# Kernel optimization log

Hardware: AMD Instinct MI355X
Metric: run time of the kernel (lower is better)

## Reference

```python
import jax, jax.numpy as jnp
import numpy as np

N, E, D, G, L = 100_000, 500_000, 128, 512, 4
BN_EPS = 1e-5

def _bn(v, g, b):
    # BatchNorm1d in training mode: biased batch stats over node/graph axis
    m = v.mean(0)
    var = v.var(0)
    return (v - m) * jax.lax.rsqrt(var + BN_EPS) * g + b

def setup_inputs() -> dict:
    key = jax.random.key(0)
    ks = jax.random.split(key, 12)
    s = 0.05
    return {
        "x": jax.random.normal(ks[0], (N, D), jnp.float32),
        "edge_index": jax.random.randint(ks[1], (2, E), 0, N, jnp.int64),
        "batch": jnp.sort(jax.random.randint(ks[2], (N,), 0, G, jnp.int64)),
        "num_graphs": G,
        "W1": jax.random.normal(ks[3], (L, D, 2 * D), jnp.float32) * s,
        "b1": jnp.zeros((L, 2 * D), jnp.float32),
        "g1": jnp.ones((L, 2 * D), jnp.float32),
        "be1": jnp.zeros((L, 2 * D), jnp.float32),
        "W2": jax.random.normal(ks[4], (L, 2 * D, D), jnp.float32) * s,
        "b2": jnp.zeros((L, D), jnp.float32),
        "gbn": jnp.ones((L, D), jnp.float32),
        "bbn": jnp.zeros((L, D), jnp.float32),
        "eps": jnp.zeros((L,), jnp.float32),
        "cW1": jax.random.normal(ks[5], (3 * D, D), jnp.float32) * s,
        "cb1": jnp.zeros((D,), jnp.float32),
        "cg": jnp.ones((D,), jnp.float32),
        "cbeta": jnp.zeros((D,), jnp.float32),
        "cW2": jax.random.normal(ks[6], (D, D // 2), jnp.float32) * s,
        "cb2": jnp.zeros((D // 2,), jnp.float32),
        "cW3": jax.random.normal(ks[7], (D // 2, 2), jnp.float32) * s,
        "cb3": jnp.zeros((2,), jnp.float32),
    }

def reference(x, edge_index, batch, num_graphs, W1, b1, g1, be1, W2, b2, gbn, bbn, eps,
              cW1, cb1, cg, cbeta, cW2, cb2, cW3, cb3):
    n = x.shape[0]
    src, dst = edge_index[0], edge_index[1]
    for l in range(W1.shape[0]):
        # GINConv: mlp((1+eps)*x + sum_{j in N(i)} x_j)  (scatter-add to dst)
        agg = jax.ops.segment_sum(x[src], dst, num_segments=n)
        h = (1.0 + eps[l]) * x + agg
        h = jax.nn.relu(_bn(h @ W1[l] + b1[l], g1[l], be1[l]))
        h = h @ W2[l] + b2[l]
        x = jax.nn.relu(_bn(h, gbn[l], bbn[l]))  # outer BN + ReLU (dropout off: eval)
    # multi-pool readout: add / mean / max per graph
    s = jax.ops.segment_sum(x, batch, num_segments=num_graphs)
    cnt = jax.ops.segment_sum(jnp.ones((n,), x.dtype), batch, num_segments=num_graphs)
    mean = s / jnp.maximum(cnt, 1.0)[:, None]
    mx = jax.ops.segment_max(x, batch, num_segments=num_graphs)
    z = jnp.concatenate([s, mean, mx], axis=-1)  # [G, 3*D]
    z = jax.nn.relu(_bn(z @ cW1 + cb1, cg, cbeta))
    z = jax.nn.relu(z @ cW2 + cb2)
    return z @ cW3 + cb3
```

## Files before the change

kernel.cpp:

```cpp
#include <hip/hip_runtime.h>
#include <cstdint>
#include <cstddef>

#define NN 100000
#define EE 500000
#define DD 128
#define GG 512
#define LL 4
#define BN_EPS 1e-5f

typedef __attribute__((ext_vector_type(8))) short short8;
typedef __attribute__((ext_vector_type(8))) unsigned short ushort8v;
typedef __attribute__((ext_vector_type(4))) float f32x4;

static __device__ __forceinline__ unsigned short f2bf(float f) {
  union { float f; unsigned u; } v;
  v.f = f;
  unsigned r = v.u + 0x7fffu + ((v.u >> 16) & 1u);
  return (unsigned short)(r >> 16);
}
static __device__ __forceinline__ float bf2f(unsigned short u) {
  union { unsigned u; float f; } v;
  v.u = ((unsigned)u) << 16;
  return v.f;
}


__global__ void k_hist(const int* __restrict__ ei, int* __restrict__ cnt) {
  int e = blockIdx.x * 256 + threadIdx.x;
  if (e < EE) {
    int d = ei[EE + e];
    if (d >= 0 && d < NN) atomicAdd(&cnt[d], 1);
  }
}

__global__ void k_part(const int* __restrict__ cnt, int* __restrict__ part) {
  __shared__ int sm[1024];
  int t = threadIdx.x;
  int i = blockIdx.x * 1024 + t;
  sm[t] = (i < NN) ? cnt[i] : 0;
  __syncthreads();
  for (int off = 512; off > 0; off >>= 1) {
    if (t < off) sm[t] += sm[t + off];
    __syncthreads();
  }
  if (t == 0) part[blockIdx.x] = sm[0];
}

__global__ void k_scanpart(const int* __restrict__ part, int* __restrict__ partx, int nb) {
  __shared__ int sm[128];
  int t = threadIdx.x;
  int v = (t < nb) ? part[t] : 0;
  sm[t] = v;
  __syncthreads();
  for (int off = 1; off < 128; off <<= 1) {
    int u = (t >= off) ? sm[t - off] : 0;
    __syncthreads();
    sm[t] += u;
    __syncthreads();
  }
  if (t < nb) partx[t] = sm[t] - v;
}

__global__ void k_rs(const int* __restrict__ cnt, const int* __restrict__ partx,
                     int* __restrict__ rs, int* __restrict__ cur) {
  __shared__ int sm[1024];
  int t = threadIdx.x;
  int i = blockIdx.x * 1024 + t;
  int v = (i < NN) ? cnt[i] : 0;
  sm[t] = v;
  __syncthreads();
  for (int off = 1; off < 1024; off <<= 1) {
    int u = (t >= off) ? sm[t - off] : 0;
    __syncthreads();
    sm[t] += u;
    __syncthreads();
  }
  if (i < NN) {
    int excl = partx[blockIdx.x] + sm[t] - v;
    rs[i] = excl;
    cur[i] = excl;
    if (i == NN - 1) rs[NN] = excl + v;
  }
}

__global__ void k_fill(const int* __restrict__ ei, int* __restrict__ cur,
                       int* __restrict__ ci) {
  int e = blockIdx.x * 256 + threadIdx.x;
  if (e < EE) {
    int s = ei[e];
    int d = ei[EE + e];
    if (d >= 0 && d < NN && s >= 0 && s < NN) {
      int pos = atomicAdd(&cur[d], 1);
      if (pos >= 0 && pos < EE) ci[pos] = s;
    }
  }
}


__global__ void k_conv(const float* __restrict__ W1, const float* __restrict__ W2,
                       unsigned short* __restrict__ W1t, unsigned short* __restrict__ W2t) {
  int idx = blockIdx.x * 256 + threadIdx.x;
  if (idx < 4 * 256 * 128) {
    {
      int l = idx >> 15, rem = idx & 32767;
      int nc = rem >> 7, k = rem & 127;
      W1t[idx] = f2bf(W1[(l << 15) + k * 256 + nc]);
    }
    {
      int l = idx >> 15, rem = idx & 32767;
      int nc = rem >> 8, k = rem & 255;
      W2t[idx] = f2bf(W2[(l << 15) + k * 128 + nc]);
    }
  }
}


__global__ void k_x2bf(const float* __restrict__ x, unsigned short* __restrict__ xb) {
  int i = blockIdx.x * 256 + threadIdx.x;
  if (i < NN * DD / 4) {
    float4 v = *(const float4*)(x + (size_t)i * 4);
    ushort4 o;
    o.x = f2bf(v.x); o.y = f2bf(v.y); o.z = f2bf(v.z); o.w = f2bf(v.w);
    *(ushort4*)(xb + (size_t)i * 4) = o;
  }
}


__global__ __launch_bounds__(256) void k_agg_bf16(
    const unsigned short* __restrict__ X, const int* __restrict__ rs,
    const int* __restrict__ ci, const float* __restrict__ epsv, int l, int mode,
    const float* __restrict__ tsc, const float* __restrict__ tsh,
    unsigned short* __restrict__ h0, int n) {
  int idx = blockIdx.x * 256 + threadIdx.x;
  int node = idx >> 4;
  int c8 = (idx & 15) << 3;
  if (node >= n) return;
  float sa[8], sb[8];
  if (mode) {
    float4 a0 = *(const float4*)(tsc + c8), a1 = *(const float4*)(tsc + c8 + 4);
    float4 b0 = *(const float4*)(tsh + c8), b1 = *(const float4*)(tsh + c8 + 4);
    sa[0] = a0.x; sa[1] = a0.y; sa[2] = a0.z; sa[3] = a0.w;
    sa[4] = a1.x; sa[5] = a1.y; sa[6] = a1.z; sa[7] = a1.w;
    sb[0] = b0.x; sb[1] = b0.y; sb[2] = b0.z; sb[3] = b0.w;
    sb[4] = b1.x; sb[5] = b1.y; sb[6] = b1.z; sb[7] = b1.w;
  }
  float se = 1.f + epsv[l];
  ushort8v v = *(const ushort8v*)(X + (size_t)node * DD + c8);
  float acc[8];
#pragma unroll
  for (int j = 0; j < 8; ++j) {
    float f = bf2f(v[j]);
    if (mode) f = fmaxf(0.f, f * sa[j] + sb[j]);
    acc[j] = se * f;
  }
  int e0 = rs[node], e1 = rs[node + 1];
  ushort8v un;
  if (e0 < e1) un = *(const ushort8v*)(X + (size_t)ci[e0] * DD + c8);
  for (int e = e0; e < e1; ++e) {
    ushort8v uc = un;
    if (e + 1 < e1) un = *(const ushort8v*)(X + (size_t)ci[e + 1] * DD + c8);
#pragma unroll
    for (int j = 0; j < 8; ++j) {
      float f = bf2f(uc[j]);
      if (mode) f = fmaxf(0.f, f * sa[j] + sb[j]);
      acc[j] += f;
    }
  }
  ushort8v o;
#pragma unroll
  for (int j = 0; j < 8; ++j) o[j] = f2bf(acc[j]);
  *(ushort8v*)(h0 + (size_t)node * DD + c8) = o;
}


__global__ __launch_bounds__(512) void k_mom(
    const unsigned short* __restrict__ h0, float* __restrict__ M2s,
    float* __restrict__ css, int n) {
  constexpr int HT = 264;
  __shared__ __align__(16) unsigned short Ht[128 * HT];
  __shared__ float lcs[128];
  int tid = threadIdx.x;
  int lane = tid & 63, wave = tid >> 6;
  int quad = lane >> 4, l15 = lane & 15;
  int n0 = blockIdx.x * 256;
  if (tid < 128) lcs[tid] = 0.f;
  int c8 = (tid & 15) << 3;
  int rloc = tid >> 4;
  float csr[8];
#pragma unroll
  for (int j = 0; j < 8; ++j) csr[j] = 0.f;
  __syncthreads();
#pragma unroll
  for (int pass = 0; pass < 8; ++pass) {
    int nl = rloc + pass * 32;
    int gr = n0 + nl;
    ushort8v v = (ushort8v){0, 0, 0, 0, 0, 0, 0, 0};
    if (gr < n) v = *(const ushort8v*)(h0 + (size_t)gr * DD + c8);
#pragma unroll
    for (int j = 0; j < 8; ++j) {
      Ht[(c8 + j) * HT + nl] = v[j];
      csr[j] += bf2f(v[j]);
    }
  }
#pragma unroll
  for (int j = 0; j < 8; ++j) atomicAdd(&lcs[c8 + j], csr[j]);
  __syncthreads();
  f32x4 acc[8];
#pragma unroll
  for (int j = 0; j < 8; ++j) acc[j] = (f32x4){0.f, 0.f, 0.f, 0.f};
#pragma unroll
  for (int kc = 0; kc < 8; ++kc) {
    int ko = kc * 32 + quad * 8;
    short8 av = *(const short8*)(&Ht[(wave * 16 + l15) * HT + ko]);
#pragma unroll
    for (int j = 0; j < 8; ++j) {
      short8 bv = *(const short8*)(&Ht[(j * 16 + l15) * HT + ko]);
      acc[j] = __builtin_amdgcn_mfma_f32_16x16x32_bf16(av, bv, acc[j], 0, 0, 0);
    }
  }
  int slab = blockIdx.x & 7;
  float* M2 = M2s + (size_t)slab * (128 * 128);
  int lr = wave * 16 + quad * 4;
#pragma unroll
  for (int j = 0; j < 8; ++j)
#pragma unroll
    for (int reg = 0; reg < 4; ++reg)
      atomicAdd(&M2[(lr + reg) * 128 + j * 16 + l15], acc[j][reg]);
  if (tid < 128) atomicAdd(&css[slab * 128 + tid], lcs[tid]);
}

__global__ void k_red(const float* __restrict__ M2s, const float* __restrict__ css,
                      float* __restrict__ M2f, float* __restrict__ csf) {
  int i = blockIdx.x * 256 + threadIdx.x;
  float s = 0.f;
#pragma unroll
  for (int k = 0; k < 8; ++k) s += M2s[(size_t)k * 16384 + i];
  M2f[i] = s;
  if (i < 128) {
    float c = 0.f;
#pragma unroll
    for (int k = 0; k < 8; ++k) c += css[k * 128 + i];
    csf[i] = c;
  }
}

__global__ __launch_bounds__(128) void k_bn1(
    const float* __restrict__ M2, const float* __restrict__ cs,
    const unsigned short* __restrict__ W1t_l, const float* __restrict__ g1_l,
    const float* __restrict__ be1_l, float* __restrict__ osc,
    float* __restrict__ osh) {
  __shared__ float wsh[128];
  __shared__ float red1[2], red2[2];
  int c = blockIdx.x, t = threadIdx.x;
  float w = bf2f(W1t_l[c * 128 + t]);
  wsh[t] = w;
  __syncthreads();
  float inner = 0.f;
#pragma unroll 4
  for (int k = 0; k < 128; ++k) inner = fmaf(M2[t * 128 + k], wsh[k], inner);
  float s1 = w * inner;
  float s2 = w * cs[t];
#pragma unroll
  for (int off = 32; off > 0; off >>= 1) {
    s1 += __shfl_xor(s1, off, 64);
    s2 += __shfl_xor(s2, off, 64);
  }
  if ((t & 63) == 0) { red1[t >> 6] = s1; red2[t >> 6] = s2; }
  __syncthreads();
  if (t == 0) {
    float q = (red1[0] + red1[1]) * (1.0f / NN);
    float um = (red2[0] + red2[1]) * (1.0f / NN);
    float var = fmaxf(q - um * um, 0.f);
    float sc = g1_l[c] * rsqrtf(var + BN_EPS);
    osc[c] = sc;
    osh[c] = be1_l[c] - um * sc;
  }
}


__global__ __launch_bounds__(512, 4) void k_gfused(
    const unsigned short* __restrict__ A, const float* __restrict__ sc1,
    const float* __restrict__ sh1, const unsigned short* __restrict__ W1t_l,
    const unsigned short* __restrict__ W2t_l, const float* __restrict__ b2_l,
    unsigned short* __restrict__ C, float* __restrict__ psum,
    float* __restrict__ psq, int n) {
  constexpr int AST = 72;
  constexpr int HP = 136;
  __shared__ __align__(16) unsigned short smem[2 * 128 * AST];
  __shared__ __align__(16) unsigned short H[128 * HP];
  __shared__ float bsum[128], bsq[128];
  unsigned short* Asm = smem;
  unsigned short* Bsm = smem + 128 * AST;

  int tid = threadIdx.x;
  int lane = tid & 63, wave = tid >> 6;
  int quad = lane >> 4, l15 = lane & 15;
  int row0 = blockIdx.x * 128;

  ushort8v pa[2], pb[2];
  f32x4 acc1[8], acc2[8];
#pragma unroll
  for (int j = 0; j < 8; ++j) acc2[j] = (f32x4){0.f, 0.f, 0.f, 0.f};

#define LOADS1(cg, kc)                                                         \
  {                                                                            \
    _Pragma("unroll") for (int it = 0; it < 2; ++it) {                         \
      int f = tid + it * 512, rr = f >> 3, c8 = (f & 7) << 3;                  \
      int gr = row0 + rr;                                                      \
      pa[it] = (ushort8v){0, 0, 0, 0, 0, 0, 0, 0};                             \
      if (gr < n)                                                              \
        pa[it] = *(const ushort8v*)(A + (size_t)gr * 128 + (kc)*64 + c8);      \
      pb[it] = *(const ushort8v*)(W1t_l +                                      \
                                  (size_t)((cg)*128 + rr) * 128 + (kc)*64 + c8); \
    }                                                                          \
  }
#define LOADS2(kc2)                                                            \
  {                                                                            \
    _Pragma("unroll") for (int it = 0; it < 2; ++it) {                         \
      int f = tid + it * 512, rr = f >> 3, c8 = (f & 7) << 3;                  \
      pb[it] = *(const ushort8v*)(W2t_l + (size_t)rr * 256 + (kc2)*64 + c8);   \
    }                                                                          \
  }
#define WRITES1                                                                \
  {                                                                            \
    _Pragma("unroll") for (int it = 0; it < 2; ++it) {                         \
      int f = tid + it * 512, rr = f >> 3, c8 = (f & 7) << 3;                  \
      *(ushort8v*)(&Asm[rr * AST + c8]) = pa[it];                              \
      *(ushort8v*)(&Bsm[rr * AST + c8]) = pb[it];                              \
    }                                                                          \
  }
#define WRITES2                                                                \
  {                                                                            \
    _Pragma("unroll") for (int it = 0; it < 2; ++it) {                         \
      int f = tid + it * 512, rr = f >> 3, c8 = (f & 7) << 3;                  \
      *(ushort8v*)(&Bsm[rr * AST + c8]) = pb[it];                              \
    }                                                                          \
  }
#define ZERO1                                                                  \
  {                                                                            \
    _Pragma("unroll") for (int j = 0; j < 8; ++j)                              \
        acc1[j] = (f32x4){0.f, 0.f, 0.f, 0.f};                                 \
  }
#define MFMAS1                                                                 \
  {                                                                            \
    _Pragma("unroll") for (int kk = 0; kk < 64; kk += 32) {                    \
      int ko = kk + quad * 8;                                                  \
      short8 av = *(const short8*)(&Asm[(wave * 16 + l15) * AST + ko]);        \
      _Pragma("unroll") for (int cf = 0; cf < 8; ++cf) {                       \
        short8 bv = *(const short8*)(&Bsm[(cf * 16 + l15) * AST + ko]);        \
        acc1[cf] =                                                             \
            __builtin_amdgcn_mfma_f32_16x16x32_bf16(av, bv, acc1[cf], 0, 0, 0); \
      }                                                                        \
    }                                                                          \
  }
#define MFMAS2(half)                                                           \
  {                                                                            \
    _Pragma("unroll") for (int kk = 0; kk < 64; kk += 32) {                    \
      int ko = kk + quad * 8;                                                  \
      short8 av =                                                              \
          *(const short8*)(&H[(wave * 16 + l15) * HP + (half)*64 + ko]);       \
      _Pragma("unroll") for (int cf = 0; cf < 8; ++cf) {                       \
        short8 bv = *(const short8*)(&Bsm[(cf * 16 + l15) * AST + ko]);        \
        acc2[cf] =                                                             \
            __builtin_amdgcn_mfma_f32_16x16x32_bf16(av, bv, acc2[cf], 0, 0, 0); \
      }                                                                        \
    }                                                                          \
  }
#define EPI1(cg)                                                               \
  {                                                                            \
    int lrb = wave * 16 + quad * 4;                                            \
    _Pragma("unroll") for (int cf = 0; cf < 8; ++cf) {                         \
      int col = (cg)*128 + cf * 16 + l15;                                      \
      float sc = sc1[col], sh = sh1[col];                                      \
      _Pragma("unroll") for (int reg = 0; reg < 4; ++reg)                      \
          H[(lrb + reg) * HP + cf * 16 + l15] =                                \
              f2bf(fmaxf(0.f, acc1[cf][reg] * sc + sh));                       \
    }                                                                          \
  }

  LOADS1(0, 0)
  WRITES1 __syncthreads();
  LOADS1(0, 1) ZERO1 MFMAS1 __syncthreads();
  WRITES1 __syncthreads();
  LOADS2(0) MFMAS1 EPI1(0) __syncthreads();
  WRITES2 __syncthreads();
  LOADS2(1) MFMAS2(0) __syncthreads();
  WRITES2 __syncthreads();
  LOADS1(1, 0) MFMAS2(1) __syncthreads();
  WRITES1 __syncthreads();
  LOADS1(1, 1) ZERO1 MFMAS1 __syncthreads();
  WRITES1 __syncthreads();
  LOADS2(2) MFMAS1 EPI1(1) __syncthreads();
  WRITES2 __syncthreads();
  LOADS2(3) MFMAS2(0) __syncthreads();
  WRITES2 __syncthreads();
  MFMAS2(1)

  __syncthreads();
  unsigned short* Ct = smem;
  if (tid < 128) { bsum[tid] = 0.f; bsq[tid] = 0.f; }
  float s8[8], q8[8];
#pragma unroll
  for (int j = 0; j < 8; ++j) { s8[j] = 0.f; q8[j] = 0.f; }
  int lrbase = wave * 16 + quad * 4;
#pragma unroll
  for (int cf = 0; cf < 8; ++cf) {
    float bv = b2_l[cf * 16 + l15];
#pragma unroll
    for (int reg = 0; reg < 4; ++reg) {
      int lr = lrbase + reg;
      float e = acc2[cf][reg] + bv;
      Ct[lr * HP + cf * 16 + l15] = f2bf(e);
      if (row0 + lr < n) { s8[cf] += e; q8[cf] += e * e; }
    }
  }
#pragma unroll
  for (int cf = 0; cf < 8; ++cf) {
    s8[cf] += __shfl_xor(s8[cf], 16, 64);
    s8[cf] += __shfl_xor(s8[cf], 32, 64);
    q8[cf] += __shfl_xor(q8[cf], 16, 64);
    q8[cf] += __shfl_xor(q8[cf], 32, 64);
  }
  __syncthreads();
  if (quad == 0) {
#pragma unroll
    for (int cf = 0; cf < 8; ++cf) {
      atomicAdd(&bsum[cf * 16 + l15], s8[cf]);
      atomicAdd(&bsq[cf * 16 + l15], q8[cf]);
    }
  }
#pragma unroll
  for (int it = 0; it < 4; ++it) {
    int f = tid + it * 512;
    int r = f >> 4, c8 = (f & 15) << 3;
    int gr = row0 + r;
    if (gr < n)
      *(ushort8v*)(C + (size_t)gr * 128 + c8) = *(const ushort8v*)(&Ct[r * HP + c8]);
  }
  __syncthreads();
  if (tid < 128) {
    psum[(size_t)blockIdx.x * 128 + tid] = bsum[tid];
    psq[(size_t)blockIdx.x * 128 + tid] = bsq[tid];
  }
#undef LOADS1
#undef LOADS2
#undef WRITES1
#undef WRITES2
#undef ZERO1
#undef MFMAS1
#undef MFMAS2
#undef EPI1
}


__global__ __launch_bounds__(256) void k_finred(
    const float* __restrict__ psum, const float* __restrict__ psq, int nb, int nc,
    const float* __restrict__ g, const float* __restrict__ be,
    float* __restrict__ osc, float* __restrict__ osh, float invn) {
  __shared__ float ws[4], wq[4];
  int col = blockIdx.x;
  int t = threadIdx.x;
  float s = 0.f, q = 0.f;
  for (int b = t; b < nb; b += 256) {
    s += psum[(size_t)b * nc + col];
    q += psq[(size_t)b * nc + col];
  }
#pragma unroll
  for (int off = 32; off > 0; off >>= 1) {
    s += __shfl_xor(s, off, 64);
    q += __shfl_xor(q, off, 64);
  }
  if ((t & 63) == 0) { ws[t >> 6] = s; wq[t >> 6] = q; }
  __syncthreads();
  if (t == 0) {
    s = ws[0] + ws[1] + ws[2] + ws[3];
    q = wq[0] + wq[1] + wq[2] + wq[3];
    float m = s * invn;
    float v = fmaxf(q * invn - m * m, 0.f);
    float sc = g[col] * rsqrtf(v + BN_EPS);
    osc[col] = sc;
    osh[col] = be[col] - m * sc;
  }
}


__global__ __launch_bounds__(256) void k_statz(
    const float* __restrict__ z1, const float* __restrict__ g,
    const float* __restrict__ be, float* __restrict__ osc, float* __restrict__ osh) {
  __shared__ float ws[4], wq[4];
  int col = blockIdx.x;
  int t = threadIdx.x;
  float s = 0.f, q = 0.f;
  for (int b = t; b < GG; b += 256) {
    float v = z1[(size_t)b * 128 + col];
    s += v;
    q += v * v;
  }
#pragma unroll
  for (int off = 32; off > 0; off >>= 1) {
    s += __shfl_xor(s, off, 64);
    q += __shfl_xor(q, off, 64);
  }
  if ((t & 63) == 0) { ws[t >> 6] = s; wq[t >> 6] = q; }
  __syncthreads();
  if (t == 0) {
    s = ws[0] + ws[1] + ws[2] + ws[3];
    q = wq[0] + wq[1] + wq[2] + wq[3];
    float m = s / (float)GG;
    float v = fmaxf(q / (float)GG - m * m, 0.f);
    float sc = g[col] * rsqrtf(v + BN_EPS);
    osc[col] = sc;
    osh[col] = be[col] - m * sc;
  }
}


static __device__ __forceinline__ int lb_i32(const int* a, int n, int key) {
  int lo = 0, hi = n;
  while (lo < hi) {
    int mid = (lo + hi) >> 1;
    if (a[mid] < key) lo = mid + 1; else hi = mid;
  }
  return lo;
}

__global__ __launch_bounds__(512) void k_pool(
    const unsigned short* __restrict__ X, const int* __restrict__ batch,
    const float* __restrict__ tsc, const float* __restrict__ tsh,
    float* __restrict__ z, int n) {
  __shared__ int slo, shi;
  __shared__ float ssum[8][128], smax[8][128];
  int g = blockIdx.x;
  int t = threadIdx.x;
  int sg = t >> 6;
  int c2 = (t & 63) << 1;
  if (t == 0) {
    slo = lb_i32(batch, n, g);
    shi = lb_i32(batch, n, g + 1);
  }
  __syncthreads();
  int lo = slo, hi = shi;
  float a0 = tsc[c2], a1 = tsc[c2 + 1];
  float b0 = tsh[c2], b1 = tsh[c2 + 1];
  float s0 = 0.f, s1 = 0.f;
  float m0 = -3.402823466e38f, m1 = -3.402823466e38f;
  for (int i = lo + sg; i < hi; i += 8) {
    unsigned u = *(const unsigned*)(X + (size_t)i * DD + c2);
    float v0 = fmaxf(0.f, bf2f((unsigned short)(u & 0xffff)) * a0 + b0);
    float v1 = fmaxf(0.f, bf2f((unsigned short)(u >> 16)) * a1 + b1);
    s0 += v0; m0 = fmaxf(m0, v0);
    s1 += v1; m1 = fmaxf(m1, v1);
  }
  ssum[sg][c2] = s0; ssum[sg][c2 + 1] = s1;
  smax[sg][c2] = m0; smax[sg][c2 + 1] = m1;
  __syncthreads();
  if (t < 128) {
    float S = 0.f, M = -3.402823466e38f;
#pragma unroll
    for (int k = 0; k < 8; ++k) {
      S += ssum[k][t];
      M = fmaxf(M, smax[k][t]);
    }
    float cntf = (float)(hi - lo);
    z[(size_t)g * 384 + t] = S;
    z[(size_t)g * 384 + 128 + t] = S / fmaxf(cntf, 1.f);
    z[(size_t)g * 384 + 256 + t] = M;
  }
}


__global__ void k_cls1(const float* __restrict__ z, const float* __restrict__ cW1,
                       const float* __restrict__ cb1, float* __restrict__ z1) {
  __shared__ float zr[384];
  int g = blockIdx.x;
  int c = threadIdx.x;
  for (int i = c; i < 384; i += 128) zr[i] = z[(size_t)g * 384 + i];
  __syncthreads();
  float s = cb1[c];
#pragma unroll 4
  for (int k = 0; k < 384; ++k) s = fmaf(zr[k], cW1[(size_t)k * 128 + c], s);
  z1[(size_t)g * 128 + c] = s;
}

__global__ void k_cls2(const float* __restrict__ z1, const float* __restrict__ csc,
                       const float* __restrict__ csh, const float* __restrict__ cW2,
                       const float* __restrict__ cb2, const float* __restrict__ cW3,
                       const float* __restrict__ cb3, float* __restrict__ out) {
  __shared__ float z1n[128];
  __shared__ float z2s[64];
  int g = blockIdx.x;
  int t = threadIdx.x;
  z1n[t] = fmaxf(0.f, z1[(size_t)g * 128 + t] * csc[t] + csh[t]);
  __syncthreads();
  if (t < 64) {
    float s = cb2[t];
#pragma unroll 4
    for (int k = 0; k < 128; ++k) s = fmaf(z1n[k], cW2[(size_t)k * 64 + t], s);
    z2s[t] = fmaxf(0.f, s);
  }
  __syncthreads();
  if (t < 2) {
    float s = cb3[t];
#pragma unroll 4
    for (int c = 0; c < 64; ++c) s = fmaf(z2s[c], cW3[(size_t)c * 2 + t], s);
    out[(size_t)g * 2 + t] = s;
  }
}


extern "C" void kernel_launch(void* const* d_in, const int* in_sizes, int n_in,
                              void* d_out, int out_size, void* d_ws, size_t ws_size,
                              hipStream_t stream) {
  const float* x = (const float*)d_in[0];
  const int* ei = (const int*)d_in[1];
  const int* batch = (const int*)d_in[2];
  const float* W1 = (const float*)d_in[4];
  const float* b1 = (const float*)d_in[5];
  const float* g1 = (const float*)d_in[6];
  const float* be1 = (const float*)d_in[7];
  const float* W2 = (const float*)d_in[8];
  const float* b2 = (const float*)d_in[9];
  const float* gbn = (const float*)d_in[10];
  const float* bbn = (const float*)d_in[11];
  const float* epsv = (const float*)d_in[12];
  const float* cW1 = (const float*)d_in[13];
  const float* cb1 = (const float*)d_in[14];
  const float* cg = (const float*)d_in[15];
  const float* cbeta = (const float*)d_in[16];
  const float* cW2 = (const float*)d_in[17];
  const float* cb2 = (const float*)d_in[18];
  const float* cW3 = (const float*)d_in[19];
  const float* cb3 = (const float*)d_in[20];
  float* out = (float*)d_out;
  (void)b1;

  char* p = (char*)d_ws;
  auto alloc = [&](size_t bytes) {
    char* r = p;
    p += (bytes + 255) & ~(size_t)255;
    return r;
  };
  const int NB = (NN + 127) / 128;
  const int NMOM = (NN + 255) / 256;
  int* cnt = (int*)alloc((size_t)NN * 4);
  int* rs = (int*)alloc((size_t)(NN + 1) * 4);
  int* cur = (int*)alloc((size_t)NN * 4);
  int* ci = (int*)alloc((size_t)EE * 4);
  int* part = (int*)alloc(128 * 4);
  int* partx = (int*)alloc(128 * 4);
  unsigned short* xbf = (unsigned short*)alloc((size_t)NN * DD * 2);
  unsigned short* h0 = (unsigned short*)alloc((size_t)NN * DD * 2);
  unsigned short* xp = (unsigned short*)alloc((size_t)NN * DD * 2);
  float* psum = (float*)alloc((size_t)NB * 128 * 4);
  float* psq = (float*)alloc((size_t)NB * 128 * 4);
  float* tsc1 = (float*)alloc(256 * 4);
  float* tsh1 = (float*)alloc(256 * 4);
  float* tscX = (float*)alloc(128 * 4);
  float* tshX = (float*)alloc(128 * 4);
  float* zbuf = (float*)alloc((size_t)GG * 384 * 4);
  float* z1 = (float*)alloc((size_t)GG * 128 * 4);
  unsigned short* W1t = (unsigned short*)alloc((size_t)4 * 256 * 128 * 2);
  unsigned short* W2t = (unsigned short*)alloc((size_t)4 * 128 * 256 * 2);
  float* mz = (float*)alloc((size_t)(8 * 128 * 128 + 8 * 128) * 4);
  float* M2s = mz;
  float* css = mz + 8 * 128 * 128;
  float* M2f = (float*)alloc((size_t)128 * 128 * 4);
  float* csf = (float*)alloc(128 * 4);
  (void)ws_size; (void)n_in; (void)in_sizes; (void)out_size;

  k_conv<<<512, 256, 0, stream>>>(W1, W2, W1t, W2t);
  k_x2bf<<<(NN * DD / 4 + 255) / 256, 256, 0, stream>>>(x, xbf);

  hipMemsetAsync(cnt, 0, (size_t)NN * 4, stream);
  k_hist<<<(EE + 255) / 256, 256, 0, stream>>>(ei, cnt);
  const int nscan = (NN + 1023) / 1024;
  k_part<<<nscan, 1024, 0, stream>>>(cnt, part);
  k_scanpart<<<1, 128, 0, stream>>>(part, partx, nscan);
  k_rs<<<nscan, 1024, 0, stream>>>(cnt, partx, rs, cur);
  k_fill<<<(EE + 255) / 256, 256, 0, stream>>>(ei, cur, ci);

  for (int l = 0; l < LL; ++l) {
    const unsigned short* Xl = (l == 0) ? xbf : xp;
    k_agg_bf16<<<(NN * 16 + 255) / 256, 256, 0, stream>>>(
        Xl, rs, ci, epsv, l, (l > 0) ? 1 : 0, tscX, tshX, h0, NN);
    hipMemsetAsync(mz, 0, (size_t)(8 * 128 * 128 + 8 * 128) * 4, stream);
    k_mom<<<NMOM, 512, 0, stream>>>(h0, M2s, css, NN);
    k_red<<<64, 256, 0, stream>>>(M2s, css, M2f, csf);
    k_bn1<<<256, 128, 0, stream>>>(M2f, csf, W1t + (size_t)l * 256 * 128,
                                   g1 + (size_t)l * 256, be1 + (size_t)l * 256,
                                   tsc1, tsh1);
    k_gfused<<<NB, 512, 0, stream>>>(
        h0, tsc1, tsh1, W1t + (size_t)l * 256 * 128, W2t + (size_t)l * 128 * 256,
        b2 + (size_t)l * 128, xp, psum, psq, NN);
    k_finred<<<128, 256, 0, stream>>>(psum, psq, NB, 128, gbn + (size_t)l * 128,
                                      bbn + (size_t)l * 128, tscX, tshX, 1.0f / NN);
  }

  k_pool<<<GG, 512, 0, stream>>>(xp, batch, tscX, tshX, zbuf, NN);
  k_cls1<<<GG, 128, 0, stream>>>(zbuf, cW1, cb1, z1);
  k_statz<<<128, 256, 0, stream>>>(z1, cg, cbeta, tscX, tshX);
  k_cls2<<<GG, 128, 0, stream>>>(z1, tscX, tshX, cW2, cb2, cW3, cb3, out);
}
```

Measured before the change: 825.8 us.

## Persistent moment kernel with per-block partials; keep A fragments in registers in fused GEMM

After: 754.8 us. 1.09x faster.

```diff
diff --git a/kernel.cpp b/kernel.cpp
--- a/kernel.cpp
+++ b/kernel.cpp
@@ -178,69 +178,78 @@
     const unsigned short* __restrict__ h0, float* __restrict__ M2s,
     float* __restrict__ css, int n) {
   constexpr int HT = 264;
+  constexpr int NCH = (NN + 255) / 256;
+  constexpr int NBLK = 196;
   __shared__ __align__(16) unsigned short Ht[128 * HT];
   __shared__ float lcs[128];
   int tid = threadIdx.x;
   int lane = tid & 63, wave = tid >> 6;
   int quad = lane >> 4, l15 = lane & 15;
-  int n0 = blockIdx.x * 256;
   if (tid < 128) lcs[tid] = 0.f;
   int c8 = (tid & 15) << 3;
   int rloc = tid >> 4;
   float csr[8];
 #pragma unroll
   for (int j = 0; j < 8; ++j) csr[j] = 0.f;
-  __syncthreads();
-#pragma unroll
-  for (int pass = 0; pass < 8; ++pass) {
-    int nl = rloc + pass * 32;
-    int gr = n0 + nl;
-    ushort8v v = (ushort8v){0, 0, 0, 0, 0, 0, 0, 0};
-    if (gr < n) v = *(const ushort8v*)(h0 + (size_t)gr * DD + c8);
-#pragma unroll
-    for (int j = 0; j < 8; ++j) {
-      Ht[(c8 + j) * HT + nl] = v[j];
-      csr[j] += bf2f(v[j]);
-    }
-  }
+  f32x4 acc[8];
+#pragma unroll
+  for (int j = 0; j < 8; ++j) acc[j] = (f32x4){0.f, 0.f, 0.f, 0.f};
+
+  for (int ch = blockIdx.x; ch < NCH; ch += NBLK) {
+    int n0 = ch * 256;
+    __syncthreads();
+#pragma unroll
+    for (int pass = 0; pass < 8; ++pass) {
+      int nl = rloc + pass * 32;
+      int gr = n0 + nl;
+      ushort8v v = (ushort8v){0, 0, 0, 0, 0, 0, 0, 0};
+      if (gr < n) v = *(const ushort8v*)(h0 + (size_t)gr * DD + c8);
+#pragma unroll
+      for (int j = 0; j < 8; ++j) {
+        int row = c8 + j;
+        int sb = (nl >> 3) ^ ((row >> 3) & 7);
+        Ht[row * HT + (sb << 3) + (nl & 7)] = v[j];
+        csr[j] += bf2f(v[j]);
+      }
+    }
+    __syncthreads();
+#pragma unroll
+    for (int kc = 0; kc < 8; ++kc) {
+      int b = kc * 4 + quad;
+      int arow = wave * 16 + l15;
+      short8 avv =
+          *(const short8*)(&Ht[arow * HT + ((b ^ ((arow >> 3) & 7)) << 3)]);
+#pragma unroll
+      for (int j = 0; j < 8; ++j) {
+        int brow = j * 16 + l15;
+        short8 bvv =
+            *(const short8*)(&Ht[brow * HT + ((b ^ ((brow >> 3) & 7)) << 3)]);
+        acc[j] = __builtin_amdgcn_mfma_f32_16x16x32_bf16(avv, bvv, acc[j], 0, 0, 0);
+      }
+    }
+  }
+  float* M2 = M2s + (size_t)blockIdx.x * 16384;
+  int lr = wave * 16 + quad * 4;
+#pragma unroll
+  for (int j = 0; j < 8; ++j)
+#pragma unroll
+    for (int g = 0; g < 4; ++g)
+      M2[(lr + g) * 128 + j * 16 + l15] = acc[j][g];
 #pragma unroll
   for (int j = 0; j < 8; ++j) atomicAdd(&lcs[c8 + j], csr[j]);
   __syncthreads();
-  f32x4 acc[8];
-#pragma unroll
-  for (int j = 0; j < 8; ++j) acc[j] = (f32x4){0.f, 0.f, 0.f, 0.f};
-#pragma unroll
-  for (int kc = 0; kc < 8; ++kc) {
-    int ko = kc * 32 + quad * 8;
-    short8 av = *(const short8*)(&Ht[(wave * 16 + l15) * HT + ko]);
-#pragma unroll
-    for (int j = 0; j < 8; ++j) {
-      short8 bv = *(const short8*)(&Ht[(j * 16 + l15) * HT + ko]);
-      acc[j] = __builtin_amdgcn_mfma_f32_16x16x32_bf16(av, bv, acc[j], 0, 0, 0);
-    }
-  }
-  int slab = blockIdx.x & 7;
-  float* M2 = M2s + (size_t)slab * (128 * 128);
-  int lr = wave * 16 + quad * 4;
-#pragma unroll
-  for (int j = 0; j < 8; ++j)
-#pragma unroll
-    for (int reg = 0; reg < 4; ++reg)
-      atomicAdd(&M2[(lr + reg) * 128 + j * 16 + l15], acc[j][reg]);
-  if (tid < 128) atomicAdd(&css[slab * 128 + tid], lcs[tid]);
+  if (tid < 128) css[(size_t)blockIdx.x * 128 + tid] = lcs[tid];
 }
 
 __global__ void k_red(const float* __restrict__ M2s, const float* __restrict__ css,
                       float* __restrict__ M2f, float* __restrict__ csf) {
   int i = blockIdx.x * 256 + threadIdx.x;
   float s = 0.f;
-#pragma unroll
-  for (int k = 0; k < 8; ++k) s += M2s[(size_t)k * 16384 + i];
+  for (int k = 0; k < 196; ++k) s += M2s[(size_t)k * 16384 + i];
   M2f[i] = s;
   if (i < 128) {
     float c = 0.f;
-#pragma unroll
-    for (int k = 0; k < 8; ++k) c += css[k * 128 + i];
+    for (int k = 0; k < 196; ++k) c += css[(size_t)k * 128 + i];
     csf[i] = c;
   }
 }
@@ -285,120 +294,111 @@
     const unsigned short* __restrict__ W2t_l, const float* __restrict__ b2_l,
     unsigned short* __restrict__ C, float* __restrict__ psum,
     float* __restrict__ psq, int n) {
-  constexpr int AST = 72;
+  constexpr int BST = 72;
   constexpr int HP = 136;
-  __shared__ __align__(16) unsigned short smem[2 * 128 * AST];
+  __shared__ __align__(16) unsigned short Bsm[2][128 * BST];
   __shared__ __align__(16) unsigned short H[128 * HP];
   __shared__ float bsum[128], bsq[128];
-  unsigned short* Asm = smem;
-  unsigned short* Bsm = smem + 128 * AST;
 
   int tid = threadIdx.x;
   int lane = tid & 63, wave = tid >> 6;
   int quad = lane >> 4, l15 = lane & 15;
   int row0 = blockIdx.x * 128;
-
-  ushort8v pa[2], pb[2];
+  int r = row0 + wave * 16 + l15;
+  bool valid = r < n;
+
+  short8 av[4];
+#pragma unroll
+  for (int ks = 0; ks < 4; ++ks) {
+    av[ks] = (short8){0, 0, 0, 0, 0, 0, 0, 0};
+    if (valid) av[ks] = *(const short8*)(A + (size_t)r * 128 + ks * 32 + quad * 8);
+  }
+
+  ushort8v pA[2], pB[2];
   f32x4 acc1[8], acc2[8];
 #pragma unroll
+  for (int j = 0; j < 8; ++j) acc1[j] = (f32x4){0.f, 0.f, 0.f, 0.f};
+#pragma unroll
   for (int j = 0; j < 8; ++j) acc2[j] = (f32x4){0.f, 0.f, 0.f, 0.f};
 
-#define LOADS1(cg, kc)                                                         \
-  {                                                                            \
-    _Pragma("unroll") for (int it = 0; it < 2; ++it) {                         \
-      int f = tid + it * 512, rr = f >> 3, c8 = (f & 7) << 3;                  \
-      int gr = row0 + rr;                                                      \
-      pa[it] = (ushort8v){0, 0, 0, 0, 0, 0, 0, 0};                             \
-      if (gr < n)                                                              \
-        pa[it] = *(const ushort8v*)(A + (size_t)gr * 128 + (kc)*64 + c8);      \
-      pb[it] = *(const ushort8v*)(W1t_l +                                      \
-                                  (size_t)((cg)*128 + rr) * 128 + (kc)*64 + c8); \
-    }                                                                          \
-  }
-#define LOADS2(kc2)                                                            \
-  {                                                                            \
-    _Pragma("unroll") for (int it = 0; it < 2; ++it) {                         \
-      int f = tid + it * 512, rr = f >> 3, c8 = (f & 7) << 3;                  \
-      pb[it] = *(const ushort8v*)(W2t_l + (size_t)rr * 256 + (kc2)*64 + c8);   \
-    }                                                                          \
-  }
-#define WRITES1                                                                \
-  {                                                                            \
-    _Pragma("unroll") for (int it = 0; it < 2; ++it) {                         \
-      int f = tid + it * 512, rr = f >> 3, c8 = (f & 7) << 3;                  \
-      *(ushort8v*)(&Asm[rr * AST + c8]) = pa[it];                              \
-      *(ushort8v*)(&Bsm[rr * AST + c8]) = pb[it];                              \
-    }                                                                          \
-  }
-#define WRITES2                                                                \
-  {                                                                            \
-    _Pragma("unroll") for (int it = 0; it < 2; ++it) {                         \
-      int f = tid + it * 512, rr = f >> 3, c8 = (f & 7) << 3;                  \
-      *(ushort8v*)(&Bsm[rr * AST + c8]) = pb[it];                              \
-    }                                                                          \
-  }
-#define ZERO1                                                                  \
-  {                                                                            \
-    _Pragma("unroll") for (int j = 0; j < 8; ++j)                              \
-        acc1[j] = (f32x4){0.f, 0.f, 0.f, 0.f};                                 \
-  }
-#define MFMAS1                                                                 \
-  {                                                                            \
-    _Pragma("unroll") for (int kk = 0; kk < 64; kk += 32) {                    \
-      int ko = kk + quad * 8;                                                  \
-      short8 av = *(const short8*)(&Asm[(wave * 16 + l15) * AST + ko]);        \
-      _Pragma("unroll") for (int cf = 0; cf < 8; ++cf) {                       \
-        short8 bv = *(const short8*)(&Bsm[(cf * 16 + l15) * AST + ko]);        \
-        acc1[cf] =                                                             \
-            __builtin_amdgcn_mfma_f32_16x16x32_bf16(av, bv, acc1[cf], 0, 0, 0); \
-      }                                                                        \
-    }                                                                          \
-  }
-#define MFMAS2(half)                                                           \
-  {                                                                            \
-    _Pragma("unroll") for (int kk = 0; kk < 64; kk += 32) {                    \
-      int ko = kk + quad * 8;                                                  \
-      short8 av =                                                              \
-          *(const short8*)(&H[(wave * 16 + l15) * HP + (half)*64 + ko]);       \
-      _Pragma("unroll") for (int cf = 0; cf < 8; ++cf) {                       \
-        short8 bv = *(const short8*)(&Bsm[(cf * 16 + l15) * AST + ko]);        \
-        acc2[cf] =                                                             \
-            __builtin_amdgcn_mfma_f32_16x16x32_bf16(av, bv, acc2[cf], 0, 0, 0); \
-      }                                                                        \
-    }                                                                          \
-  }
-#define EPI1(cg)                                                               \
-  {                                                                            \
-    int lrb = wave * 16 + quad * 4;                                            \
-    _Pragma("unroll") for (int cf = 0; cf < 8; ++cf) {                         \
-      int col = (cg)*128 + cf * 16 + l15;                                      \
-      float sc = sc1[col], sh = sh1[col];                                      \
-      _Pragma("unroll") for (int reg = 0; reg < 4; ++reg)                      \
-          H[(lrb + reg) * HP + cf * 16 + l15] =                                \
-              f2bf(fmaxf(0.f, acc1[cf][reg] * sc + sh));                       \
-    }                                                                          \
-  }
-
-  LOADS1(0, 0)
-  WRITES1 __syncthreads();
-  LOADS1(0, 1) ZERO1 MFMAS1 __syncthreads();
-  WRITES1 __syncthreads();
-  LOADS2(0) MFMAS1 EPI1(0) __syncthreads();
-  WRITES2 __syncthreads();
-  LOADS2(1) MFMAS2(0) __syncthreads();
-  WRITES2 __syncthreads();
-  LOADS1(1, 0) MFMAS2(1) __syncthreads();
-  WRITES1 __syncthreads();
-  LOADS1(1, 1) ZERO1 MFMAS1 __syncthreads();
-  WRITES1 __syncthreads();
-  LOADS2(2) MFMAS1 EPI1(1) __syncthreads();
-  WRITES2 __syncthreads();
-  LOADS2(3) MFMAS2(0) __syncthreads();
-  WRITES2 __syncthreads();
-  MFMAS2(1)
-
-  __syncthreads();
-  unsigned short* Ct = smem;
+#define LD_W1(dst, cg, kc)                                                      \
+  {                                                                             \
+    _Pragma("unroll") for (int it = 0; it < 2; ++it) {                          \
+      int f = tid + it * 512, rr = f >> 3, cc = (f & 7) << 3;                   \
+      dst[it] = *(const ushort8v*)(W1t_l + (size_t)((cg)*128 + rr) * 128 +      \
+                                   (kc)*64 + cc);                               \
+    }                                                                           \
+  }
+#define LD_W2(dst, kc2)                                                         \
+  {                                                                             \
+    _Pragma("unroll") for (int it = 0; it < 2; ++it) {                          \
+      int f = tid + it * 512, rr = f >> 3, cc = (f & 7) << 3;                   \
+      dst[it] = *(const ushort8v*)(W2t_l + (size_t)rr * 256 + (kc2)*64 + cc);   \
+    }                                                                           \
+  }
+#define ST_B(buf, src)                                                          \
+  {                                                                             \
+    _Pragma("unroll") for (int it = 0; it < 2; ++it) {                          \
+      int f = tid + it * 512, rr = f >> 3, cc = (f & 7) << 3;                   \
+      *(ushort8v*)(&Bsm[buf][rr * BST + cc]) = src[it];                         \
+    }                                                                           \
+  }
+#define MM1(buf, k2)                                                            \
+  {                                                                             \
+    _Pragma("unroll") for (int kk = 0; kk < 2; ++kk) {                          \
+      int ko = kk * 32 + quad * 8;                                              \
+      short8 a = av[(k2)*2 + kk];                                               \
+      _Pragma("unroll") for (int cf = 0; cf < 8; ++cf) {                        \
+        short8 bv = *(const short8*)(&Bsm[buf][(cf * 16 + l15) * BST + ko]);    \
+        acc1[cf] = __builtin_amdgcn_mfma_f32_16x16x32_bf16(a, bv, acc1[cf],     \
+                                                           0, 0, 0);            \
+      }                                                                         \
+    }                                                                           \
+  }
+#define MM2(buf, half)                                                          \
+  {                                                                             \
+    _Pragma("unroll") for (int kk = 0; kk < 64; kk += 32) {                     \
+      int ko = kk + quad * 8;                                                   \
+      short8 a = *(const short8*)(&H[(wave * 16 + l15) * HP + (half)*64 + ko]); \
+      _Pragma("unroll") for (int cf = 0; cf < 8; ++cf) {                        \
+        short8 bv = *(const short8*)(&Bsm[buf][(cf * 16 + l15) * BST + ko]);    \
+        acc2[cf] = __builtin_amdgcn_mfma_f32_16x16x32_bf16(a, bv, acc2[cf],     \
+                                                           0, 0, 0);            \
+      }                                                                         \
+    }                                                                           \
+  }
+#define EPI(cg)                                                                 \
+  {                                                                             \
+    int lrb = wave * 16 + quad * 4;                                             \
+    _Pragma("unroll") for (int cf = 0; cf < 8; ++cf) {                          \
+      int col = (cg)*128 + cf * 16 + l15;                                       \
+      float sc = sc1[col], sh = sh1[col];                                       \
+      _Pragma("unroll") for (int g = 0; g < 4; ++g)                             \
+          H[(lrb + g) * HP + cf * 16 + l15] =                                   \
+              f2bf(fmaxf(0.f, acc1[cf][g] * sc + sh));                          \
+    }                                                                           \
+  }
+#define ZACC1                                                                   \
+  {                                                                             \
+    _Pragma("unroll") for (int j = 0; j < 8; ++j)                               \
+        acc1[j] = (f32x4){0.f, 0.f, 0.f, 0.f};                                  \
+  }
+
+  LD_W1(pA, 0, 0)
+  LD_W1(pB, 0, 1)
+  ST_B(0, pA)
+  __syncthreads();
+  LD_W2(pA, 0) MM1(0, 0) ST_B(1, pB) __syncthreads();
+  LD_W2(pB, 1) MM1(1, 1) EPI(0) ST_B(0, pA) __syncthreads();
+  LD_W1(pA, 1, 0) MM2(0, 0) ST_B(1, pB) __syncthreads();
+  LD_W1(pB, 1, 1) MM2(1, 1) ST_B(0, pA) __syncthreads();
+  LD_W2(pA, 2) ZACC1 MM1(0, 0) ST_B(1, pB) __syncthreads();
+  LD_W2(pB, 3) MM1(1, 1) EPI(1) ST_B(0, pA) __syncthreads();
+  MM2(0, 0) ST_B(1, pB) __syncthreads();
+  MM2(1, 1)
+
+  __syncthreads();
+  unsigned short* Ct = H;
   if (tid < 128) { bsum[tid] = 0.f; bsq[tid] = 0.f; }
   float s8[8], q8[8];
 #pragma unroll
@@ -408,9 +408,9 @@
   for (int cf = 0; cf < 8; ++cf) {
     float bv = b2_l[cf * 16 + l15];
 #pragma unroll
-    for (int reg = 0; reg < 4; ++reg) {
-      int lr = lrbase + reg;
-      float e = acc2[cf][reg] + bv;
+    for (int g = 0; g < 4; ++g) {
+      int lr = lrbase + g;
+      float e = acc2[cf][g] + bv;
       Ct[lr * HP + cf * 16 + l15] = f2bf(e);
       if (row0 + lr < n) { s8[cf] += e; q8[cf] += e * e; }
     }
@@ -433,24 +433,23 @@
 #pragma unroll
   for (int it = 0; it < 4; ++it) {
     int f = tid + it * 512;
-    int r = f >> 4, c8 = (f & 15) << 3;
-    int gr = row0 + r;
+    int rr = f >> 4, cc = (f & 15) << 3;
+    int gr = row0 + rr;
     if (gr < n)
-      *(ushort8v*)(C + (size_t)gr * 128 + c8) = *(const ushort8v*)(&Ct[r * HP + c8]);
+      *(ushort8v*)(C + (size_t)gr * 128 + cc) = *(const ushort8v*)(&Ct[rr * HP + cc]);
   }
   __syncthreads();
   if (tid < 128) {
     psum[(size_t)blockIdx.x * 128 + tid] = bsum[tid];
     psq[(size_t)blockIdx.x * 128 + tid] = bsq[tid];
   }
-#undef LOADS1
-#undef LOADS2
-#undef WRITES1
-#undef WRITES2
-#undef ZERO1
-#undef MFMAS1
-#undef MFMAS2
-#undef EPI1
+#undef LD_W1
+#undef LD_W2
+#undef ST_B
+#undef MM1
+#undef MM2
+#undef EPI
+#undef ZACC1
 }
 
 
@@ -642,7 +641,6 @@
     return r;
   };
   const int NB = (NN + 127) / 128;
-  const int NMOM = (NN + 255) / 256;
   int* cnt = (int*)alloc((size_t)NN * 4);
   int* rs = (int*)alloc((size_t)(NN + 1) * 4);
   int* cur = (int*)alloc((size_t)NN * 4);
@@ -662,9 +660,8 @@
   float* z1 = (float*)alloc((size_t)GG * 128 * 4);
   unsigned short* W1t = (unsigned short*)alloc((size_t)4 * 256 * 128 * 2);
   unsigned short* W2t = (unsigned short*)alloc((size_t)4 * 128 * 256 * 2);
-  float* mz = (float*)alloc((size_t)(8 * 128 * 128 + 8 * 128) * 4);
-  float* M2s = mz;
-  float* css = mz + 8 * 128 * 128;
+  float* M2s = (float*)alloc((size_t)196 * 16384 * 4);
+  float* css = (float*)alloc((size_t)196 * 128 * 4);
   float* M2f = (float*)alloc((size_t)128 * 128 * 4);
   float* csf = (float*)alloc(128 * 4);
   (void)ws_size; (void)n_in; (void)in_sizes; (void)out_size;
@@ -684,8 +681,7 @@
     const unsigned short* Xl = (l == 0) ? xbf : xp;
     k_agg_bf16<<<(NN * 16 + 255) / 256, 256, 0, stream>>>(
         Xl, rs, ci, epsv, l, (l > 0) ? 1 : 0, tscX, tshX, h0, NN);
-    hipMemsetAsync(mz, 0, (size_t)(8 * 128 * 128 + 8 * 128) * 4, stream);
-    k_mom<<<NMOM, 512, 0, stream>>>(h0, M2s, css, NN);
+    k_mom<<<196, 512, 0, stream>>>(h0, M2s, css, NN);
     k_red<<<64, 256, 0, stream>>>(M2s, css, M2f, csf);
     k_bn1<<<256, 128, 0, stream>>>(M2f, csf, W1t + (size_t)l * 256 * 128,
                                    g1 + (size_t)l * 256, be1 + (size_t)l * 256,
```
